# Optimization experiments

Measured on AMD Instinct MI355X. Metric: run time of the kernel, lower is better.

## Reference

```python
import jax, jax.numpy as jnp
import numpy as np

DIM = 1024
HEADS = 16
HEAD_DIM = DIM // HEADS
DECAY = 0.95
EPS = 1e-5


def setup_inputs() -> dict:
    key = jax.random.key(0)
    ks = jax.random.split(key, 11)
    B, S, D = 2, 2048, DIM
    s = 1.0 / np.sqrt(D)
    inp = {
        'x': jax.random.normal(ks[0], (B, S, D), dtype=jnp.float32),
        'Wq': jax.random.normal(ks[1], (D, D), dtype=jnp.float32) * s,
        'bq': jnp.zeros((D,), jnp.float32),
        'Wk': jax.random.normal(ks[2], (D, D), dtype=jnp.float32) * s,
        'bk': jnp.zeros((D,), jnp.float32),
        'Wv': jax.random.normal(ks[3], (D, D), dtype=jnp.float32) * s,
        'bv': jnp.zeros((D,), jnp.float32),
        'Wo': jax.random.normal(ks[4], (D, D), dtype=jnp.float32) * s,
        'bo': jnp.zeros((D,), jnp.float32),
        'gamma': jnp.ones((D,), jnp.float32),
        'beta': jnp.zeros((D,), jnp.float32),
    }
    return inp


def _decay_mask(S, dtype):
    idx = jnp.arange(S)
    diff = (idx[:, None] - idx[None, :]).astype(jnp.float32)
    # decay^(i-j) for i >= j, else 0
    mask = jnp.where(diff >= 0, jnp.exp(diff * np.log(DECAY)), 0.0)
    return mask.astype(dtype)


def reference(x, Wq, bq, Wk, bk, Wv, bv, Wo, bo, gamma, beta):
    B, S, D = x.shape
    H, hd = HEADS, HEAD_DIM

    def split_heads(y):  # [B,S,D] -> [B,H,S,hd]
        return y.reshape(B, S, H, hd).transpose(0, 2, 1, 3)

    q = split_heads(x @ Wq + bq)
    k = split_heads(x @ Wk + bk)
    v = split_heads(x @ Wv + bv)

    mask = _decay_mask(S, x.dtype)  # [S,S]
    scores = jnp.einsum('bhid,bhjd->bhij', q, k) * mask
    out = jnp.einsum('bhij,bhjd->bhid', scores, v)  # [B,H,S,hd]

    out = out.transpose(0, 2, 1, 3).reshape(B, S, D)
    out = out @ Wo + bo

    # GroupNorm(H groups) applied over channel dim with seq as spatial dim
    y = out.transpose(0, 2, 1)            # [B,D,S]
    yg = y.reshape(B, H, hd, S)
    mu = yg.mean(axis=(2, 3), keepdims=True)
    var = yg.var(axis=(2, 3), keepdims=True)
    yn = (yg - mu) / jnp.sqrt(var + EPS)
    yn = yn.reshape(B, D, S) * gamma[None, :, None] + beta[None, :, None]
    return yn.transpose(0, 2, 1)          # [B,S,D]
```

## Files before the change

kernel.cpp:

```cpp
#include <hip/hip_runtime.h>
#include <hip/hip_bf16.h>

typedef unsigned short u16;
typedef __attribute__((ext_vector_type(8))) short short8;
typedef __attribute__((ext_vector_type(4))) float f32x4;
typedef __attribute__((ext_vector_type(4))) unsigned short u16x4;

#define SEQ 2048
#define NH 16
#define HD 64
#define DM 1024
#define LN_DECAY (-0.051293294387550536f)
#define WIN_TILES 4

__device__ __forceinline__ float b2f(u16 u) {
    return __uint_as_float(((unsigned int)u) << 16);
}
__device__ __forceinline__ u16 f2b(float f) {
    unsigned int u = __float_as_uint(f);
    u += 0x7fffu + ((u >> 16) & 1u);
    return (u16)(u >> 16);
}
__device__ __forceinline__ f32x4 mfma16(short8 a, short8 b, f32x4 c) {
    return __builtin_amdgcn_mfma_f32_16x16x32_bf16(a, b, c, 0, 0, 0);
}
__device__ __forceinline__ void gld_lds16(const u16* g, u16* l) {
    __builtin_amdgcn_global_load_lds(
        (const __attribute__((address_space(1))) void*)g,
        (__attribute__((address_space(3))) void*)l, 16, 0, 0);
}
__device__ __forceinline__ int detect_fl(const u16* Wq, int lane) {
    int hit = 0;
#pragma unroll
    for (int j = 0; j < 4; j++) {
        u16 u = Wq[2*(lane + 64*j)];
        if (((u >> 7) & 0xFF) >= 0xC0) hit = 1;
    }
    return (__ballot(hit) != 0ULL) ? 1 : 0;
}

__global__ __launch_bounds__(256) void prep(
    const void* __restrict__ x,
    const void* __restrict__ Wq, const void* __restrict__ Wk,
    const void* __restrict__ Wv, const void* __restrict__ Wo,
    const void* __restrict__ bq, const void* __restrict__ bk,
    const void* __restrict__ bv, const void* __restrict__ bo,
    const void* __restrict__ gamma, const void* __restrict__ beta,
    u16* __restrict__ xc,
    u16* __restrict__ WqT, u16* __restrict__ WkT,
    u16* __restrict__ WvT, u16* __restrict__ WoT,
    u16* __restrict__ bqc, u16* __restrict__ bkc, u16* __restrict__ bvc,
    u16* __restrict__ boc, u16* __restrict__ gammac, u16* __restrict__ betac,
    int* __restrict__ flag, float* __restrict__ statsAcc)
{
    __shared__ u16 tileS[32][33];
    int bid = blockIdx.x, tid = threadIdx.x;
    int fl = detect_fl((const u16*)Wq, tid & 63);

    if (bid < 4096) {
        int i = (bid*256 + tid)*4;
        if (fl) {
            f32x4 v = *(const f32x4*)((const float*)x + i);
            u16x4 o = { f2b(v[0]), f2b(v[1]), f2b(v[2]), f2b(v[3]) };
            *(u16x4*)(xc + i) = o;
        } else {
            *(u16x4*)(xc + i) = *(const u16x4*)((const u16*)x + i);
        }
    } else if (bid == 4096) {
        const void* ins[6] = {bq, bk, bv, bo, gamma, beta};
        u16* outs[6] = {bqc, bkc, bvc, boc, gammac, betac};
        int i = tid*4;
#pragma unroll
        for (int a = 0; a < 6; a++) {
            if (fl) {
                f32x4 v = *(const f32x4*)((const float*)ins[a] + i);
                u16x4 o = { f2b(v[0]), f2b(v[1]), f2b(v[2]), f2b(v[3]) };
                *(u16x4*)(outs[a] + i) = o;
            } else {
                *(u16x4*)(outs[a] + i) = *(const u16x4*)((const u16*)ins[a] + i);
            }
        }
        if (tid == 0) *flag = fl;
        if (tid < 64) statsAcc[tid] = 0.f;
    } else {
        int tb = bid - 4097;
        int wsel = tb >> 10, tile = tb & 1023;
        const void* W = (wsel==0) ? Wq : (wsel==1) ? Wk : (wsel==2) ? Wv : Wo;
        u16* T        = (wsel==0) ? WqT : (wsel==1) ? WkT : (wsel==2) ? WvT : WoT;
        int bn = (tile & 31)*32, bk_ = (tile >> 5)*32;
        int r = tid >> 5, c = tid & 31;
#pragma unroll
        for (int i2 = 0; i2 < 4; i2++) {
            size_t idx = (size_t)(bk_ + r + i2*8)*DM + bn + c;
            tileS[r + i2*8][c] = fl ? f2b(((const float*)W)[idx]) : ((const u16*)W)[idx];
        }
        __syncthreads();
#pragma unroll
        for (int i2 = 0; i2 < 4; i2++)
            T[(size_t)(bn + r + i2*8)*DM + bk_ + c] = tileS[c][r + i2*8];
    }
}

template<int MODE>
__device__ __forceinline__ void gemm_body(
    const u16* __restrict__ A, const u16* __restrict__ BT,
    const u16* __restrict__ bias, u16* __restrict__ outB,
    float* __restrict__ outF, float* __restrict__ stats,
    int m0, int n0, int t)
{
    __shared__ u16 As[128*32];
    __shared__ u16 Bs[128*32];
    int w = t >> 6, l = t & 63;
    int lane16 = l & 15, quad = l >> 4;
    int wm = (w >> 1) * 64, wn = (w & 1) * 64;

    int srow   = t >> 2;
    int schunk = (t & 3) ^ ((t >> 3) & 3);

    f32x4 zero = {0.f, 0.f, 0.f, 0.f};
    f32x4 acc[4][4];
#pragma unroll
    for (int i = 0; i < 4; i++)
#pragma unroll
        for (int j = 0; j < 4; j++)
            acc[i][j] = zero;

    const u16* a0 = A  + (size_t)(m0 + srow)      * DM + schunk*8;
    const u16* a1 = A  + (size_t)(m0 + srow + 64) * DM + schunk*8;
    const u16* b0 = BT + (size_t)(n0 + srow)      * DM + schunk*8;
    const u16* b1 = BT + (size_t)(n0 + srow + 64) * DM + schunk*8;

    for (int k0 = 0; k0 < DM; k0 += 32) {
        __syncthreads();
        gld_lds16(a0 + k0, &As[t*8]);
        gld_lds16(a1 + k0, &As[2048 + t*8]);
        gld_lds16(b0 + k0, &Bs[t*8]);
        gld_lds16(b1 + k0, &Bs[2048 + t*8]);
        __syncthreads();
        short8 af[4], bf[4];
#pragma unroll
        for (int i = 0; i < 4; i++) {
            int ra = wm + i*16 + lane16;
            int rb = wn + i*16 + lane16;
            af[i] = *(const short8*)(&As[ra*32 + ((quad ^ ((ra>>1)&3))*8)]);
            bf[i] = *(const short8*)(&Bs[rb*32 + ((quad ^ ((rb>>1)&3))*8)]);
        }
#pragma unroll
        for (int i = 0; i < 4; i++)
#pragma unroll
            for (int j = 0; j < 4; j++)
                acc[i][j] = mfma16(af[i], bf[j], acc[i][j]);
    }

    float s = 0.f, ss = 0.f;
#pragma unroll
    for (int i = 0; i < 4; i++) {
#pragma unroll
        for (int j = 0; j < 4; j++) {
            int n = n0 + wn + j*16 + lane16;
            float bv = b2f(bias[n]);
#pragma unroll
            for (int r = 0; r < 4; r++) {
                int m = m0 + wm + i*16 + quad*4 + r;
                float v = acc[i][j][r] + bv;
                if (MODE == 3) {
                    outF[(size_t)m*DM + n] = v;
                    s += v; ss += v*v;
                } else {
                    int b = m >> 11, sq = m & (SEQ-1);
                    int h = n >> 6,  d = n & (HD-1);
                    if (MODE == 2)
                        outB[(((size_t)(b*NH + h))*HD + d)*SEQ + sq] = f2b(v);
                    else
                        outB[(((size_t)(b*NH + h))*SEQ + sq)*HD + d] = f2b(v);
                }
            }
        }
    }
    if (MODE == 3) {
#pragma unroll
        for (int off = 32; off > 0; off >>= 1) {
            s  += __shfl_down(s, off);
            ss += __shfl_down(ss, off);
        }
        if (l == 0) {
            int b = m0 >> 11;
            int g = (n0 + wn) >> 6;
            atomicAdd(&stats[(b*NH + g)*2],     s);
            atomicAdd(&stats[(b*NH + g)*2 + 1], ss);
        }
    }
}

__global__ __launch_bounds__(256) void gemm_qkv(
    const u16* __restrict__ x,
    const u16* __restrict__ WqT, const u16* __restrict__ WkT, const u16* __restrict__ WvT,
    const u16* __restrict__ bq, const u16* __restrict__ bk, const u16* __restrict__ bv,
    u16* __restrict__ qb, u16* __restrict__ kb, u16* __restrict__ vTb)
{
    int z = blockIdx.z;
    const u16* BT   = (z==0) ? WqT : (z==1) ? WkT : WvT;
    const u16* bias = (z==0) ? bq  : (z==1) ? bk  : bv;
    u16* outB       = (z==0) ? qb  : (z==1) ? kb  : vTb;
    if (z == 2)
        gemm_body<2>(x, BT, bias, outB, nullptr, nullptr,
                     blockIdx.x * 128, blockIdx.y * 128, threadIdx.x);
    else
        gemm_body<0>(x, BT, bias, outB, nullptr, nullptr,
                     blockIdx.x * 128, blockIdx.y * 128, threadIdx.x);
}

__global__ __launch_bounds__(256) void gemm_out(
    const u16* __restrict__ attn, const u16* __restrict__ WoT,
    const u16* __restrict__ bo, float* __restrict__ proj,
    float* __restrict__ statsAcc)
{
    gemm_body<3>(attn, WoT, bo, nullptr, proj, statsAcc,
                 blockIdx.x * 128, blockIdx.y * 128, threadIdx.x);
}

__global__ __launch_bounds__(256) void retention(
    const u16* __restrict__ q, const u16* __restrict__ k,
    const u16* __restrict__ vT, u16* __restrict__ attn)
{
    __shared__ u16 Ks[64*64];
    __shared__ u16 Vs[64*64];
    __shared__ u16 Ps[4][16*64];

    int qt = blockIdx.x, bh = blockIdx.y;
    int t = threadIdx.x, w = t >> 6, l = t & 63;
    int c = l & 15, qd = l >> 4;
    int qbase = qt * 64;
    int iwave = qbase + w*16;

    const u16* qh = q  + (size_t)bh * SEQ * HD;
    const u16* kh = k  + (size_t)bh * SEQ * HD;
    const u16* vh = vT + (size_t)bh * HD * SEQ;

    float D[4], E[4];
#pragma unroll
    for (int r = 0; r < 4; r++)
        D[r] = __expf((float)(qd*4 + r) * LN_DECAY);
#pragma unroll
    for (int st = 0; st < 4; st++)
        E[st] = __expf(-(float)(st*16 + c) * LN_DECAY);

    int sr = t >> 3, sc8 = t & 7;

    short8 qf[2];
#pragma unroll
    for (int kk = 0; kk < 2; kk++)
        qf[kk] = *(const short8*)(qh + (size_t)(iwave + c)*HD + kk*32 + qd*8);

    f32x4 zero = {0.f, 0.f, 0.f, 0.f};
    f32x4 oacc[4] = {zero, zero, zero, zero};

    int jt0 = (qt > WIN_TILES) ? (qt - WIN_TILES) : 0;
#pragma unroll 1
    for (int jt = jt0; jt <= qt; jt++) {
        int jbase = jt * 64;
        __syncthreads();
        {
            int r0 = sr, r1 = sr + 32;
            *(short8*)(&Ks[r0*64 + ((sc8 ^ (r0&7))*8)]) = *(const short8*)(kh + (size_t)(jbase+r0)*HD + sc8*8);
            *(short8*)(&Ks[r1*64 + ((sc8 ^ (r1&7))*8)]) = *(const short8*)(kh + (size_t)(jbase+r1)*HD + sc8*8);
            *(short8*)(&Vs[r0*64 + ((sc8 ^ (r0&7))*8)]) = *(const short8*)(vh + (size_t)r0*SEQ + jbase + sc8*8);
            *(short8*)(&Vs[r1*64 + ((sc8 ^ (r1&7))*8)]) = *(const short8*)(vh + (size_t)(r1)*SEQ + jbase + sc8*8);
        }
        __syncthreads();

        f32x4 sacc[4] = {zero, zero, zero, zero};
#pragma unroll
        for (int kk = 0; kk < 2; kk++) {
#pragma unroll
            for (int st = 0; st < 4; st++) {
                int row = st*16 + c;
                short8 bf = *(const short8*)(&Ks[row*64 + (((kk*4+qd) ^ (row&7))*8)]);
                sacc[st] = mfma16(qf[kk], bf, sacc[st]);
            }
        }

        float base = __expf((float)(iwave - jbase) * LN_DECAY);
#pragma unroll
        for (int st = 0; st < 4; st++) {
            int j = jbase + st*16 + c;
            float bE = base * E[st];
#pragma unroll
            for (int r = 0; r < 4; r++) {
                int i = iwave + qd*4 + r;
                float val = (i >= j) ? sacc[st][r] * (bE * D[r]) : 0.0f;
                int row = qd*4 + r;
                int col = st*16 + c;
                Ps[w][row*64 + (((col>>3) ^ (row&7))*8) + (col&7)] = f2b(val);
            }
        }
        asm volatile("s_waitcnt lgkmcnt(0)" ::: "memory");
        short8 pf[2];
#pragma unroll
        for (int kk = 0; kk < 2; kk++)
            pf[kk] = *(const short8*)(&Ps[w][c*64 + (((kk*4+qd) ^ (c&7))*8)]);

#pragma unroll
        for (int kk = 0; kk < 2; kk++) {
#pragma unroll
            for (int nt = 0; nt < 4; nt++) {
                int row = nt*16 + c;
                short8 vf = *(const short8*)(&Vs[row*64 + (((kk*4+qd) ^ (row&7))*8)]);
                oacc[nt] = mfma16(pf[kk], vf, oacc[nt]);
            }
        }
    }

    int b = bh >> 4, h = bh & (NH-1);
#pragma unroll
    for (int nt = 0; nt < 4; nt++) {
        int d = h*HD + nt*16 + c;
#pragma unroll
        for (int r = 0; r < 4; r++) {
            int s = iwave + qd*4 + r;
            attn[((size_t)(b*SEQ + s))*DM + d] = f2b(oacc[nt][r]);
        }
    }
}

__global__ __launch_bounds__(256) void gn_apply(
    const float* __restrict__ proj, const float* __restrict__ statsAcc,
    const u16* __restrict__ gamma, const u16* __restrict__ beta,
    const int* __restrict__ flag, void* __restrict__ outv)
{
    int base = (blockIdx.x*256 + threadIdx.x)*4;
    int d = base & (DM-1);
    int b = base >> 21;
    int g = d >> 6;
    float S  = statsAcc[(b*NH + g)*2];
    float SS = statsAcc[(b*NH + g)*2 + 1];
    const float inv = 1.0f/(float)(SEQ*HD);
    float mu = S*inv;
    float rstd = rsqrtf(SS*inv - mu*mu + 1e-5f);
    f32x4 v = *(const f32x4*)(proj + base);
    float o0 = (v[0]-mu)*rstd*b2f(gamma[d])   + b2f(beta[d]);
    float o1 = (v[1]-mu)*rstd*b2f(gamma[d+1]) + b2f(beta[d+1]);
    float o2 = (v[2]-mu)*rstd*b2f(gamma[d+2]) + b2f(beta[d+2]);
    float o3 = (v[3]-mu)*rstd*b2f(gamma[d+3]) + b2f(beta[d+3]);
    if (*flag) {
        f32x4 ov = {o0, o1, o2, o3};
        *(f32x4*)((float*)outv + base) = ov;
    } else {
        u16x4 ov = {f2b(o0), f2b(o1), f2b(o2), f2b(o3)};
        *(u16x4*)((u16*)outv + base) = ov;
    }
}

extern "C" void kernel_launch(void* const* d_in, const int* in_sizes, int n_in,
                              void* d_out, int out_size, void* d_ws, size_t ws_size,
                              hipStream_t stream) {
    const void* x     = d_in[0];
    const void* Wq    = d_in[1];
    const void* bq    = d_in[2];
    const void* Wk    = d_in[3];
    const void* bk    = d_in[4];
    const void* Wv    = d_in[5];
    const void* bv    = d_in[6];
    const void* Wo    = d_in[7];
    const void* bo    = d_in[8];
    const void* gamma = d_in[9];
    const void* beta  = d_in[10];

    const size_t MB = 1024*1024;
    char* ws = (char*)d_ws;
    int*   flag     = (int*)ws;
    u16*   bqc      = (u16*)(ws + 4096);
    u16*   bkc      = (u16*)(ws + 8192);
    u16*   bvc      = (u16*)(ws + 12288);
    u16*   boc      = (u16*)(ws + 16384);
    u16*   gammac   = (u16*)(ws + 20480);
    u16*   betac    = (u16*)(ws + 24576);
    float* statsAcc = (float*)(ws + 28672);
    u16*   xc     = (u16*)(ws + 1*MB);
    u16*   WqT    = (u16*)(ws + 9*MB);
    u16*   WkT    = (u16*)(ws + 11*MB);
    u16*   WvT    = (u16*)(ws + 13*MB);
    u16*   WoT    = (u16*)(ws + 15*MB);
    u16*   qb     = (u16*)(ws + 17*MB);
    u16*   kb     = (u16*)(ws + 25*MB);
    u16*   vTb    = (u16*)(ws + 33*MB);
    u16*   attn   = (u16*)(ws + 41*MB);
    float* proj   = (float*)(ws + 17*MB);

    prep<<<8193, 256, 0, stream>>>(x, Wq, Wk, Wv, Wo, bq, bk, bv, bo, gamma, beta,
                                   xc, WqT, WkT, WvT, WoT,
                                   bqc, bkc, bvc, boc, gammac, betac,
                                   flag, statsAcc);
    gemm_qkv<<<dim3(32, 8, 3), 256, 0, stream>>>(xc, WqT, WkT, WvT, bqc, bkc, bvc, qb, kb, vTb);
    retention<<<dim3(32, 32), 256, 0, stream>>>(qb, kb, vTb, attn);
    gemm_out<<<dim3(32, 8), 256, 0, stream>>>(attn, WoT, boc, proj, statsAcc);
    gn_apply<<<4096, 256, 0, stream>>>(proj, statsAcc, gammac, betac, flag, d_out);
}
```

Baseline: 184.4 us.

## Fuse output projection and GroupNorm with cooperative grid sync

Merges the output projection GEMM and the GroupNorm apply kernel into one cooperative kernel. Each block keeps its accumulators in registers, adds its partial group statistics atomically, waits on a grid-wide sync, then normalizes and writes the final output directly. This removes the fp32 round trip of the projection buffer through global memory and one kernel launch. In exchange it adds a grid barrier and requires all 256 blocks to be co-resident, which a cooperative launch enforces.

```diff
diff --git a/kernel.cpp b/kernel.cpp
--- a/kernel.cpp
+++ b/kernel.cpp
@@ -1,5 +1,8 @@
 #include <hip/hip_runtime.h>
 #include <hip/hip_bf16.h>
+#include <hip/hip_cooperative_groups.h>
+
+namespace cg = cooperative_groups;
 
 typedef unsigned short u16;
 typedef __attribute__((ext_vector_type(8))) short short8;
@@ -101,24 +104,19 @@
     }
 }
 
-template<int MODE>
-__device__ __forceinline__ void gemm_body(
+__device__ __forceinline__ void gemm_core(
     const u16* __restrict__ A, const u16* __restrict__ BT,
-    const u16* __restrict__ bias, u16* __restrict__ outB,
-    float* __restrict__ outF, float* __restrict__ stats,
-    int m0, int n0, int t)
+    u16* As, u16* Bs, int m0, int n0, int t, f32x4 (&acc)[4][4])
 {
-    __shared__ u16 As[128*32];
-    __shared__ u16 Bs[128*32];
-    int w = t >> 6, l = t & 63;
+    int l = t & 63;
     int lane16 = l & 15, quad = l >> 4;
+    int w = t >> 6;
     int wm = (w >> 1) * 64, wn = (w & 1) * 64;
 
     int srow   = t >> 2;
     int schunk = (t & 3) ^ ((t >> 3) & 3);
 
     f32x4 zero = {0.f, 0.f, 0.f, 0.f};
-    f32x4 acc[4][4];
 #pragma unroll
     for (int i = 0; i < 4; i++)
 #pragma unroll
@@ -151,45 +149,6 @@
             for (int j = 0; j < 4; j++)
                 acc[i][j] = mfma16(af[i], bf[j], acc[i][j]);
     }
-
-    float s = 0.f, ss = 0.f;
-#pragma unroll
-    for (int i = 0; i < 4; i++) {
-#pragma unroll
-        for (int j = 0; j < 4; j++) {
-            int n = n0 + wn + j*16 + lane16;
-            float bv = b2f(bias[n]);
-#pragma unroll
-            for (int r = 0; r < 4; r++) {
-                int m = m0 + wm + i*16 + quad*4 + r;
-                float v = acc[i][j][r] + bv;
-                if (MODE == 3) {
-                    outF[(size_t)m*DM + n] = v;
-                    s += v; ss += v*v;
-                } else {
-                    int b = m >> 11, sq = m & (SEQ-1);
-                    int h = n >> 6,  d = n & (HD-1);
-                    if (MODE == 2)
-                        outB[(((size_t)(b*NH + h))*HD + d)*SEQ + sq] = f2b(v);
-                    else
-                        outB[(((size_t)(b*NH + h))*SEQ + sq)*HD + d] = f2b(v);
-                }
-            }
-        }
-    }
-    if (MODE == 3) {
-#pragma unroll
-        for (int off = 32; off > 0; off >>= 1) {
-            s  += __shfl_down(s, off);
-            ss += __shfl_down(ss, off);
-        }
-        if (l == 0) {
-            int b = m0 >> 11;
-            int g = (n0 + wn) >> 6;
-            atomicAdd(&stats[(b*NH + g)*2],     s);
-            atomicAdd(&stats[(b*NH + g)*2 + 1], ss);
-        }
-    }
 }
 
 __global__ __launch_bounds__(256) void gemm_qkv(
@@ -198,25 +157,38 @@
     const u16* __restrict__ bq, const u16* __restrict__ bk, const u16* __restrict__ bv,
     u16* __restrict__ qb, u16* __restrict__ kb, u16* __restrict__ vTb)
 {
+    __shared__ u16 As[128*32];
+    __shared__ u16 Bs[128*32];
     int z = blockIdx.z;
     const u16* BT   = (z==0) ? WqT : (z==1) ? WkT : WvT;
     const u16* bias = (z==0) ? bq  : (z==1) ? bk  : bv;
     u16* outB       = (z==0) ? qb  : (z==1) ? kb  : vTb;
-    if (z == 2)
-        gemm_body<2>(x, BT, bias, outB, nullptr, nullptr,
-                     blockIdx.x * 128, blockIdx.y * 128, threadIdx.x);
-    else
-        gemm_body<0>(x, BT, bias, outB, nullptr, nullptr,
-                     blockIdx.x * 128, blockIdx.y * 128, threadIdx.x);
-}
-
-__global__ __launch_bounds__(256) void gemm_out(
-    const u16* __restrict__ attn, const u16* __restrict__ WoT,
-    const u16* __restrict__ bo, float* __restrict__ proj,
-    float* __restrict__ statsAcc)
-{
-    gemm_body<3>(attn, WoT, bo, nullptr, proj, statsAcc,
-                 blockIdx.x * 128, blockIdx.y * 128, threadIdx.x);
+    int m0 = blockIdx.x * 128, n0 = blockIdx.y * 128, t = threadIdx.x;
+
+    f32x4 acc[4][4];
+    gemm_core(x, BT, As, Bs, m0, n0, t, acc);
+
+    int l = t & 63, lane16 = l & 15, quad = l >> 4, w = t >> 6;
+    int wm = (w >> 1) * 64, wn = (w & 1) * 64;
+#pragma unroll
+    for (int i = 0; i < 4; i++) {
+#pragma unroll
+        for (int j = 0; j < 4; j++) {
+            int n = n0 + wn + j*16 + lane16;
+            float bvv = b2f(bias[n]);
+#pragma unroll
+            for (int r = 0; r < 4; r++) {
+                int m = m0 + wm + i*16 + quad*4 + r;
+                float v = acc[i][j][r] + bvv;
+                int b = m >> 11, sq = m & (SEQ-1);
+                int h = n >> 6,  d = n & (HD-1);
+                if (z == 2)
+                    outB[(((size_t)(b*NH + h))*HD + d)*SEQ + sq] = f2b(v);
+                else
+                    outB[(((size_t)(b*NH + h))*SEQ + sq)*HD + d] = f2b(v);
+            }
+        }
+    }
 }
 
 __global__ __launch_bounds__(256) void retention(
@@ -323,31 +295,74 @@
     }
 }
 
-__global__ __launch_bounds__(256) void gn_apply(
-    const float* __restrict__ proj, const float* __restrict__ statsAcc,
-    const u16* __restrict__ gamma, const u16* __restrict__ beta,
-    const int* __restrict__ flag, void* __restrict__ outv)
+__global__ __launch_bounds__(256) void gemm_out_gn(
+    const u16* __restrict__ attn, const u16* __restrict__ WoT,
+    const u16* __restrict__ bo, const u16* __restrict__ gamma,
+    const u16* __restrict__ beta, const int* __restrict__ flag,
+    float* __restrict__ stats, void* __restrict__ outv)
 {
-    int base = (blockIdx.x*256 + threadIdx.x)*4;
-    int d = base & (DM-1);
-    int b = base >> 21;
-    int g = d >> 6;
-    float S  = statsAcc[(b*NH + g)*2];
-    float SS = statsAcc[(b*NH + g)*2 + 1];
+    __shared__ u16 As[128*32];
+    __shared__ u16 Bs[128*32];
+    int m0 = blockIdx.x * 128, n0 = blockIdx.y * 128, t = threadIdx.x;
+
+    f32x4 acc[4][4];
+    gemm_core(attn, WoT, As, Bs, m0, n0, t, acc);
+
+    int l = t & 63, lane16 = l & 15, quad = l >> 4, w = t >> 6;
+    int wm = (w >> 1) * 64, wn = (w & 1) * 64;
+
+    float s = 0.f, ss = 0.f;
+#pragma unroll
+    for (int i = 0; i < 4; i++) {
+#pragma unroll
+        for (int j = 0; j < 4; j++) {
+            int n = n0 + wn + j*16 + lane16;
+            float bvv = b2f(bo[n]);
+#pragma unroll
+            for (int r = 0; r < 4; r++) {
+                float v = acc[i][j][r] + bvv;
+                acc[i][j][r] = v;
+                s += v; ss += v*v;
+            }
+        }
+    }
+#pragma unroll
+    for (int off = 32; off > 0; off >>= 1) {
+        s  += __shfl_down(s, off);
+        ss += __shfl_down(ss, off);
+    }
+    int b = m0 >> 11;
+    int g = (n0 + wn) >> 6;
+    if (l == 0) {
+        atomicAdd(&stats[(b*NH + g)*2],     s);
+        atomicAdd(&stats[(b*NH + g)*2 + 1], ss);
+    }
+    __threadfence();
+    cg::this_grid().sync();
+
+    float S  = __hip_atomic_load(&stats[(b*NH + g)*2],
+                                 __ATOMIC_RELAXED, __HIP_MEMORY_SCOPE_AGENT);
+    float SS = __hip_atomic_load(&stats[(b*NH + g)*2 + 1],
+                                 __ATOMIC_RELAXED, __HIP_MEMORY_SCOPE_AGENT);
     const float inv = 1.0f/(float)(SEQ*HD);
     float mu = S*inv;
     float rstd = rsqrtf(SS*inv - mu*mu + 1e-5f);
-    f32x4 v = *(const f32x4*)(proj + base);
-    float o0 = (v[0]-mu)*rstd*b2f(gamma[d])   + b2f(beta[d]);
-    float o1 = (v[1]-mu)*rstd*b2f(gamma[d+1]) + b2f(beta[d+1]);
-    float o2 = (v[2]-mu)*rstd*b2f(gamma[d+2]) + b2f(beta[d+2]);
-    float o3 = (v[3]-mu)*rstd*b2f(gamma[d+3]) + b2f(beta[d+3]);
-    if (*flag) {
-        f32x4 ov = {o0, o1, o2, o3};
-        *(f32x4*)((float*)outv + base) = ov;
-    } else {
-        u16x4 ov = {f2b(o0), f2b(o1), f2b(o2), f2b(o3)};
-        *(u16x4*)((u16*)outv + base) = ov;
+    int fl = *flag;
+#pragma unroll
+    for (int i = 0; i < 4; i++) {
+#pragma unroll
+        for (int j = 0; j < 4; j++) {
+            int n = n0 + wn + j*16 + lane16;
+            float gm = b2f(gamma[n]);
+            float bt = b2f(beta[n]);
+#pragma unroll
+            for (int r = 0; r < 4; r++) {
+                int m = m0 + wm + i*16 + quad*4 + r;
+                float o = (acc[i][j][r] - mu)*rstd*gm + bt;
+                if (fl) ((float*)outv)[(size_t)m*DM + n] = o;
+                else    ((u16*)outv)[(size_t)m*DM + n] = f2b(o);
+            }
+        }
     }
 }
 
@@ -385,7 +400,6 @@
     u16*   kb     = (u16*)(ws + 25*MB);
     u16*   vTb    = (u16*)(ws + 33*MB);
     u16*   attn   = (u16*)(ws + 41*MB);
-    float* proj   = (float*)(ws + 17*MB);
 
     prep<<<8193, 256, 0, stream>>>(x, Wq, Wk, Wv, Wo, bq, bk, bv, bo, gamma, beta,
                                    xc, WqT, WkT, WvT, WoT,
@@ -393,6 +407,19 @@
                                    flag, statsAcc);
     gemm_qkv<<<dim3(32, 8, 3), 256, 0, stream>>>(xc, WqT, WkT, WvT, bqc, bkc, bvc, qb, kb, vTb);
     retention<<<dim3(32, 32), 256, 0, stream>>>(qb, kb, vTb, attn);
-    gemm_out<<<dim3(32, 8), 256, 0, stream>>>(attn, WoT, boc, proj, statsAcc);
-    gn_apply<<<4096, 256, 0, stream>>>(proj, statsAcc, gammac, betac, flag, d_out);
-}
+    {
+        const u16* attn_  = attn;
+        const u16* WoT_   = WoT;
+        const u16* bo_    = boc;
+        const u16* gamma_ = gammac;
+        const u16* beta_  = betac;
+        const int* flag_  = flag;
+        float*     stats_ = statsAcc;
+        void*      out_   = d_out;
+        void* kargs[] = { (void*)&attn_, (void*)&WoT_, (void*)&bo_,
+                          (void*)&gamma_, (void*)&beta_, (void*)&flag_,
+                          (void*)&stats_, (void*)&out_ };
+        hipLaunchCooperativeKernel(gemm_out_gn, dim3(32, 8), dim3(256, 1, 1),
+                                   kargs, 0, stream);
+    }
+}
```

New measurement: 254.5 us. +38.0%, slower.

## Split output projection over K into two partial GEMMs with separate GroupNorm stats pass

Applied to the files above, without the earlier changes.

The output projection GEMM now runs as two K-halves (split-K over 512 each) writing separate fp32 partial buffers, doubling the grid from 256 to 512 blocks for better CU occupancy. Bias addition and GroupNorm statistics move out of the GEMM epilogue into a new gn_stats kernel that sums the partials, and gn_apply also reads both partials plus the bias. This trades an extra kernel launch and extra fp32 traffic (two 8MB partial buffers read twice) for more parallelism in the projection GEMM and fewer atomics in its epilogue.

```diff
diff --git a/kernel.cpp b/kernel.cpp
--- a/kernel.cpp
+++ b/kernel.cpp
@@ -101,24 +101,20 @@
     }
 }
 
-template<int MODE>
-__device__ __forceinline__ void gemm_body(
+template<int KLEN>
+__device__ __forceinline__ void gemm_core(
     const u16* __restrict__ A, const u16* __restrict__ BT,
-    const u16* __restrict__ bias, u16* __restrict__ outB,
-    float* __restrict__ outF, float* __restrict__ stats,
-    int m0, int n0, int t)
-{
-    __shared__ u16 As[128*32];
-    __shared__ u16 Bs[128*32];
-    int w = t >> 6, l = t & 63;
+    u16* As, u16* Bs, int m0, int n0, int t, f32x4 (&acc)[4][4])
+{
+    int l = t & 63;
     int lane16 = l & 15, quad = l >> 4;
+    int w = t >> 6;
     int wm = (w >> 1) * 64, wn = (w & 1) * 64;
 
     int srow   = t >> 2;
     int schunk = (t & 3) ^ ((t >> 3) & 3);
 
     f32x4 zero = {0.f, 0.f, 0.f, 0.f};
-    f32x4 acc[4][4];
 #pragma unroll
     for (int i = 0; i < 4; i++)
 #pragma unroll
@@ -130,7 +126,7 @@
     const u16* b0 = BT + (size_t)(n0 + srow)      * DM + schunk*8;
     const u16* b1 = BT + (size_t)(n0 + srow + 64) * DM + schunk*8;
 
-    for (int k0 = 0; k0 < DM; k0 += 32) {
+    for (int k0 = 0; k0 < KLEN; k0 += 32) {
         __syncthreads();
         gld_lds16(a0 + k0, &As[t*8]);
         gld_lds16(a1 + k0, &As[2048 + t*8]);
@@ -151,45 +147,6 @@
             for (int j = 0; j < 4; j++)
                 acc[i][j] = mfma16(af[i], bf[j], acc[i][j]);
     }
-
-    float s = 0.f, ss = 0.f;
-#pragma unroll
-    for (int i = 0; i < 4; i++) {
-#pragma unroll
-        for (int j = 0; j < 4; j++) {
-            int n = n0 + wn + j*16 + lane16;
-            float bv = b2f(bias[n]);
-#pragma unroll
-            for (int r = 0; r < 4; r++) {
-                int m = m0 + wm + i*16 + quad*4 + r;
-                float v = acc[i][j][r] + bv;
-                if (MODE == 3) {
-                    outF[(size_t)m*DM + n] = v;
-                    s += v; ss += v*v;
-                } else {
-                    int b = m >> 11, sq = m & (SEQ-1);
-                    int h = n >> 6,  d = n & (HD-1);
-                    if (MODE == 2)
-                        outB[(((size_t)(b*NH + h))*HD + d)*SEQ + sq] = f2b(v);
-                    else
-                        outB[(((size_t)(b*NH + h))*SEQ + sq)*HD + d] = f2b(v);
-                }
-            }
-        }
-    }
-    if (MODE == 3) {
-#pragma unroll
-        for (int off = 32; off > 0; off >>= 1) {
-            s  += __shfl_down(s, off);
-            ss += __shfl_down(ss, off);
-        }
-        if (l == 0) {
-            int b = m0 >> 11;
-            int g = (n0 + wn) >> 6;
-            atomicAdd(&stats[(b*NH + g)*2],     s);
-            atomicAdd(&stats[(b*NH + g)*2 + 1], ss);
-        }
-    }
 }
 
 __global__ __launch_bounds__(256) void gemm_qkv(
@@ -198,25 +155,38 @@
     const u16* __restrict__ bq, const u16* __restrict__ bk, const u16* __restrict__ bv,
     u16* __restrict__ qb, u16* __restrict__ kb, u16* __restrict__ vTb)
 {
+    __shared__ u16 As[128*32];
+    __shared__ u16 Bs[128*32];
     int z = blockIdx.z;
     const u16* BT   = (z==0) ? WqT : (z==1) ? WkT : WvT;
     const u16* bias = (z==0) ? bq  : (z==1) ? bk  : bv;
     u16* outB       = (z==0) ? qb  : (z==1) ? kb  : vTb;
-    if (z == 2)
-        gemm_body<2>(x, BT, bias, outB, nullptr, nullptr,
-                     blockIdx.x * 128, blockIdx.y * 128, threadIdx.x);
-    else
-        gemm_body<0>(x, BT, bias, outB, nullptr, nullptr,
-                     blockIdx.x * 128, blockIdx.y * 128, threadIdx.x);
-}
-
-__global__ __launch_bounds__(256) void gemm_out(
-    const u16* __restrict__ attn, const u16* __restrict__ WoT,
-    const u16* __restrict__ bo, float* __restrict__ proj,
-    float* __restrict__ statsAcc)
-{
-    gemm_body<3>(attn, WoT, bo, nullptr, proj, statsAcc,
-                 blockIdx.x * 128, blockIdx.y * 128, threadIdx.x);
+    int m0 = blockIdx.x * 128, n0 = blockIdx.y * 128, t = threadIdx.x;
+
+    f32x4 acc[4][4];
+    gemm_core<DM>(x, BT, As, Bs, m0, n0, t, acc);
+
+    int l = t & 63, lane16 = l & 15, quad = l >> 4, w = t >> 6;
+    int wm = (w >> 1) * 64, wn = (w & 1) * 64;
+#pragma unroll
+    for (int i = 0; i < 4; i++) {
+#pragma unroll
+        for (int j = 0; j < 4; j++) {
+            int n = n0 + wn + j*16 + lane16;
+            float bvv = b2f(bias[n]);
+#pragma unroll
+            for (int r = 0; r < 4; r++) {
+                int m = m0 + wm + i*16 + quad*4 + r;
+                float v = acc[i][j][r] + bvv;
+                int b = m >> 11, sq = m & (SEQ-1);
+                int h = n >> 6,  d = n & (HD-1);
+                if (z == 2)
+                    outB[(((size_t)(b*NH + h))*HD + d)*SEQ + sq] = f2b(v);
+                else
+                    outB[(((size_t)(b*NH + h))*SEQ + sq)*HD + d] = f2b(v);
+            }
+        }
+    }
 }
 
 __global__ __launch_bounds__(256) void retention(
@@ -323,8 +293,74 @@
     }
 }
 
+__global__ __launch_bounds__(256) void gemm_out(
+    const u16* __restrict__ attn, const u16* __restrict__ WoT,
+    float* __restrict__ proj0, float* __restrict__ proj1)
+{
+    __shared__ u16 As[128*32];
+    __shared__ u16 Bs[128*32];
+    int z = blockIdx.z;
+    const u16* A  = attn + (z ? 512 : 0);
+    const u16* BT = WoT  + (z ? 512 : 0);
+    float* proj   = z ? proj1 : proj0;
+    int m0 = blockIdx.x * 128, n0 = blockIdx.y * 128, t = threadIdx.x;
+
+    f32x4 acc[4][4];
+    gemm_core<512>(A, BT, As, Bs, m0, n0, t, acc);
+
+    int l = t & 63, lane16 = l & 15, quad = l >> 4, w = t >> 6;
+    int wm = (w >> 1) * 64, wn = (w & 1) * 64;
+#pragma unroll
+    for (int i = 0; i < 4; i++) {
+#pragma unroll
+        for (int j = 0; j < 4; j++) {
+            int n = n0 + wn + j*16 + lane16;
+#pragma unroll
+            for (int r = 0; r < 4; r++) {
+                int m = m0 + wm + i*16 + quad*4 + r;
+                proj[(size_t)m*DM + n] = acc[i][j][r];
+            }
+        }
+    }
+}
+
+__global__ __launch_bounds__(256) void gn_stats(
+    const float* __restrict__ proj0, const float* __restrict__ proj1,
+    const u16* __restrict__ bo, float* __restrict__ statsAcc)
+{
+    int bg = blockIdx.x >> 3;
+    int ch = blockIdx.x & 7;
+    int b  = bg >> 4, g = bg & 15;
+    int t = threadIdx.x;
+    int col = g*64 + (t & 15)*4;
+    float bo0 = b2f(bo[col]),   bo1 = b2f(bo[col+1]);
+    float bo2 = b2f(bo[col+2]), bo3 = b2f(bo[col+3]);
+    int rbase = b*SEQ + ch*256;
+    float s = 0.f, ss = 0.f;
+#pragma unroll 4
+    for (int r = t >> 4; r < 256; r += 16) {
+        size_t idx = (size_t)(rbase + r)*DM + col;
+        f32x4 v0 = *(const f32x4*)(proj0 + idx);
+        f32x4 v1 = *(const f32x4*)(proj1 + idx);
+        float a0 = v0[0]+v1[0]+bo0; s += a0; ss += a0*a0;
+        float a1 = v0[1]+v1[1]+bo1; s += a1; ss += a1*a1;
+        float a2 = v0[2]+v1[2]+bo2; s += a2; ss += a2*a2;
+        float a3 = v0[3]+v1[3]+bo3; s += a3; ss += a3*a3;
+    }
+#pragma unroll
+    for (int off = 32; off > 0; off >>= 1) {
+        s  += __shfl_down(s, off);
+        ss += __shfl_down(ss, off);
+    }
+    if ((t & 63) == 0) {
+        atomicAdd(&statsAcc[bg*2],     s);
+        atomicAdd(&statsAcc[bg*2 + 1], ss);
+    }
+}
+
 __global__ __launch_bounds__(256) void gn_apply(
-    const float* __restrict__ proj, const float* __restrict__ statsAcc,
+    const float* __restrict__ proj0, const float* __restrict__ proj1,
+    const float* __restrict__ statsAcc, const u16* __restrict__ bo,
     const u16* __restrict__ gamma, const u16* __restrict__ beta,
     const int* __restrict__ flag, void* __restrict__ outv)
 {
@@ -337,11 +373,16 @@
     const float inv = 1.0f/(float)(SEQ*HD);
     float mu = S*inv;
     float rstd = rsqrtf(SS*inv - mu*mu + 1e-5f);
-    f32x4 v = *(const f32x4*)(proj + base);
-    float o0 = (v[0]-mu)*rstd*b2f(gamma[d])   + b2f(beta[d]);
-    float o1 = (v[1]-mu)*rstd*b2f(gamma[d+1]) + b2f(beta[d+1]);
-    float o2 = (v[2]-mu)*rstd*b2f(gamma[d+2]) + b2f(beta[d+2]);
-    float o3 = (v[3]-mu)*rstd*b2f(gamma[d+3]) + b2f(beta[d+3]);
+    f32x4 v0 = *(const f32x4*)(proj0 + base);
+    f32x4 v1 = *(const f32x4*)(proj1 + base);
+    float c0 = v0[0]+v1[0]+b2f(bo[d]);
+    float c1 = v0[1]+v1[1]+b2f(bo[d+1]);
+    float c2 = v0[2]+v1[2]+b2f(bo[d+2]);
+    float c3 = v0[3]+v1[3]+b2f(bo[d+3]);
+    float o0 = (c0-mu)*rstd*b2f(gamma[d])   + b2f(beta[d]);
+    float o1 = (c1-mu)*rstd*b2f(gamma[d+1]) + b2f(beta[d+1]);
+    float o2 = (c2-mu)*rstd*b2f(gamma[d+2]) + b2f(beta[d+2]);
+    float o3 = (c3-mu)*rstd*b2f(gamma[d+3]) + b2f(beta[d+3]);
     if (*flag) {
         f32x4 ov = {o0, o1, o2, o3};
         *(f32x4*)((float*)outv + base) = ov;
@@ -385,7 +426,8 @@
     u16*   kb     = (u16*)(ws + 25*MB);
     u16*   vTb    = (u16*)(ws + 33*MB);
     u16*   attn   = (u16*)(ws + 41*MB);
-    float* proj   = (float*)(ws + 17*MB);
+    float* proj0  = (float*)(ws + 17*MB);
+    float* proj1  = (float*)(ws + 49*MB);
 
     prep<<<8193, 256, 0, stream>>>(x, Wq, Wk, Wv, Wo, bq, bk, bv, bo, gamma, beta,
                                    xc, WqT, WkT, WvT, WoT,
@@ -393,6 +435,7 @@
                                    flag, statsAcc);
     gemm_qkv<<<dim3(32, 8, 3), 256, 0, stream>>>(xc, WqT, WkT, WvT, bqc, bkc, bvc, qb, kb, vTb);
     retention<<<dim3(32, 32), 256, 0, stream>>>(qb, kb, vTb, attn);
-    gemm_out<<<dim3(32, 8), 256, 0, stream>>>(attn, WoT, boc, proj, statsAcc);
-    gn_apply<<<4096, 256, 0, stream>>>(proj, statsAcc, gammac, betac, flag, d_out);
-}
+    gemm_out<<<dim3(32, 8, 2), 256, 0, stream>>>(attn, WoT, proj0, proj1);
+    gn_stats<<<256, 256, 0, stream>>>(proj0, proj1, boc, statsAcc);
+    gn_apply<<<4096, 256, 0, stream>>>(proj0, proj1, statsAcc, boc, gammac, betac, flag, d_out);
+}
```

Result: slower. 194.8 us (+5.6%).
